# Kernel tuning notes

Hardware: AMD Instinct MI355X
Metric: run time of the kernel (lower is better)

The kernel has to match this reference:

```python
import jax, jax.numpy as jnp
import numpy as np

N_NODES = 7
SIZE_X = 27
SIZE_X0 = 23
SIZE_H = 1024
SIZE_Z = 256
BATCH = 2048


def _gru(x, h, Wih, Whh, bih, bhh):
    # torch.nn.GRUCell math
    gi = x @ Wih.T + bih          # [B, 3H]
    gh = h @ Whh.T + bhh          # [B, 3H]
    ir, iz, inn = jnp.split(gi, 3, axis=-1)
    hr, hz, hn = jnp.split(gh, 3, axis=-1)
    r = jax.nn.sigmoid(ir + hr)
    z = jax.nn.sigmoid(iz + hz)
    n = jnp.tanh(inn + r * hn)
    return (1.0 - z) * n + z * h


def setup_inputs() -> dict:
    key = jax.random.key(0)
    ks = jax.random.split(key, 24)
    H, Xd, X0d, Zd = SIZE_H, SIZE_X, SIZE_X0, SIZE_Z

    def w(k, shape, fan):
        return jax.random.normal(k, shape, jnp.float32) / np.float32(np.sqrt(fan))

    inp = {}
    inp['X'] = jax.random.normal(ks[0], (BATCH, N_NODES, Xd), jnp.float32)
    inp['adj'] = jax.random.randint(ks[1], (BATCH, N_NODES, N_NODES), 0, 2, jnp.int32)
    # combin_encode GRUCell
    inp['W_ih_c'] = w(ks[2], (3 * H, Xd), H)
    inp['W_hh_c'] = w(ks[3], (3 * H, H), H)
    inp['b_ih_c'] = w(ks[4], (3 * H,), H)
    inp['b_hh_c'] = w(ks[5], (3 * H,), H)
    # loop_encode GRUCell
    inp['W_ih_l'] = w(ks[6], (3 * H, Xd), H)
    inp['W_hh_l'] = w(ks[7], (3 * H, H), H)
    inp['b_ih_l'] = w(ks[8], (3 * H,), H)
    inp['b_hh_l'] = w(ks[9], (3 * H,), H)
    # root_encode GRUCell (input size = size_X0)
    inp['W_ih_r'] = w(ks[10], (3 * H, X0d), H)
    inp['W_hh_r'] = w(ks[11], (3 * H, H), H)
    inp['b_ih_r'] = w(ks[12], (3 * H,), H)
    inp['b_hh_r'] = w(ks[13], (3 * H,), H)
    # gate: Linear(2H -> H) + sigmoid ; mapper: Linear(2H -> H, no bias)
    inp['Wg'] = w(ks[14], (H, 2 * H), 2 * H)
    inp['bg'] = w(ks[15], (H,), 2 * H)
    inp['Wm'] = w(ks[16], (H, 2 * H), 2 * H)
    # h_to_mu, h_to_std (Linear(H -> Z), std with softplus)
    inp['Wmu'] = w(ks[17], (Zd, H), H)
    inp['bmu'] = w(ks[18], (Zd,), H)
    inp['Wstd'] = w(ks[19], (Zd, H), H)
    inp['bstd'] = w(ks[20], (Zd,), H)
    return inp


def reference(X, adj,
              W_ih_c, W_hh_c, b_ih_c, b_hh_c,
              W_ih_l, W_hh_l, b_ih_l, b_hh_l,
              W_ih_r, W_hh_r, b_ih_r, b_hh_r,
              Wg, bg, Wm, Wmu, bmu, Wstd, bstd):
    B = X.shape[0]
    hidden = jnp.zeros((B, N_NODES, SIZE_H), X.dtype)
    # encode: nodes processed v = n-1 .. 0 (fixed small unrolled loop)
    for v in range(N_NODES - 1, -1, -1):
        if v == N_NODES - 1:
            H_in = jnp.zeros((B, SIZE_H), X.dtype)  # H_init = zeros
        else:
            H_nb = hidden[:, v + 1:, :]                    # [B, k, H] neighbors v+1..n-1
            pred = (adj[:, v + 1:, v] > 0)[..., None]       # edge x -> v
            succ = (adj[:, v, v + 1:] > 0)[..., None]       # edge v -> x
            Hcat = jnp.concatenate([jnp.where(pred, H_nb, 0.0),
                                    jnp.where(succ, H_nb, 0.0)], axis=-1)  # [B, k, 2H]
            g = jax.nn.sigmoid(jnp.einsum('bkf,hf->bkh', Hcat, Wg) + bg)
            m = jnp.einsum('bkf,hf->bkh', Hcat, Wm)
            H_in = (g * m).sum(axis=1)                      # gated sum over neighbors
        Xv = X[:, v]
        if v == 0:
            Hv = _gru(Xv[:, :SIZE_X0], H_in, W_ih_r, W_hh_r, b_ih_r, b_hh_r)
        else:
            Hv = _gru(Xv, H_in, W_ih_c, W_hh_c, b_ih_c, b_hh_c)
            self_loop = (adj[:, v, v] > 0)[:, None]
            X_loop = jnp.where(self_loop, Xv, 0.0)
            Hv = _gru(X_loop, Hv, W_ih_l, W_hh_l, b_ih_l, b_hh_l)
        hidden = hidden.at[:, v].set(Hv)
    Hg = hidden[:, 0]
    mu = Hg @ Wmu.T + bmu
    std = jax.nn.softplus(Hg @ Wstd.T + bstd)
    return mu, std
```

## Files before the change

### kernel.cpp

```cpp
#include <hip/hip_runtime.h>
#include <hip/hip_bf16.h>
#include <cmath>


typedef __hip_bfloat16 bf16;
typedef __attribute__((ext_vector_type(8))) short bf16x8;
typedef __attribute__((ext_vector_type(4))) float f32x4;

constexpr int BATCH = 2048;
constexpr int HD    = 1024;
constexpr int LDA   = 1056;
constexpr size_t BH = (size_t)BATCH * HD;

__device__ __forceinline__ bf16  f2bf(float v){ return __float2bfloat16(v); }
__device__ __forceinline__ float sigm(float x){ return 1.0f/(1.0f+__expf(-x)); }

__device__ __forceinline__ void async16(bf16* lds_wave_uniform, const bf16* g){
  __builtin_amdgcn_global_load_lds(
      (const __attribute__((address_space(1))) void*)g,
      (__attribute__((address_space(3))) void*)lds_wave_uniform, 16, 0, 0);
}
__device__ __forceinline__ void ld4f(const bf16* p, float* o){
  ushort4 u = *reinterpret_cast<const ushort4*>(p);
  o[0] = __uint_as_float(((unsigned)u.x)<<16);
  o[1] = __uint_as_float(((unsigned)u.y)<<16);
  o[2] = __uint_as_float(((unsigned)u.z)<<16);
  o[3] = __uint_as_float(((unsigned)u.w)<<16);
}
__device__ __forceinline__ void st4bf(bf16* p, const float* v){
  bf16 o[4] = {f2bf(v[0]), f2bf(v[1]), f2bf(v[2]), f2bf(v[3])};
  *reinterpret_cast<ushort4*>(p) = *reinterpret_cast<const ushort4*>(o);
}

__global__ __launch_bounds__(256) void pack_waug_i(
    const float* __restrict__ Whh, const float* __restrict__ Wih, int xw,
    bf16* __restrict__ out)
{
  int c = blockIdx.x;
  int h = c >> 2, g = c & 3;
  for (int ch = threadIdx.x; ch < 264; ch += 256){
    int f0 = ch*4;
    float v[4] = {0.f,0.f,0.f,0.f};
    if (f0 < 1024){
      if (g < 3){
        int src = (g==2) ? (2048+h) : (g*1024+h);
        const float4 t = *reinterpret_cast<const float4*>(Whh + (size_t)src*1024 + f0);
        v[0]=t.x; v[1]=t.y; v[2]=t.z; v[3]=t.w;
      }
    } else if (g != 2){
      int src = (g==0) ? h : (g==1) ? (1024+h) : (2048+h);
      int fx = f0 - 1024;
      #pragma unroll
      for (int j=0;j<4;++j) if (fx+j < xw) v[j] = Wih[(size_t)src*xw + fx + j];
    }
    st4bf(out + (size_t)c*LDA + f0, v);
  }
}

__global__ __launch_bounds__(256) void pack_wgm(const float* __restrict__ Wg,
    const float* __restrict__ Wm, bf16* __restrict__ outW){
  int i = blockIdx.x*256 + threadIdx.x;
  int c = i >> 8, f0 = (i & 255)*4;
  int j = c >> 10, h = c & 1023;
  const float* src = (j < 2) ? Wg : Wm;
  float4 t = *reinterpret_cast<const float4*>(src + (size_t)h*2048 + ((j & 1) ? 1024 : 0) + f0);
  float v[4] = {t.x,t.y,t.z,t.w};
  st4bf(outW + (size_t)c*1024 + f0, v);
}

__global__ __launch_bounds__(256) void pack_wms(const float* __restrict__ Wmu,
    const float* __restrict__ Wstd, bf16* __restrict__ outW){
  int i = blockIdx.x*256 + threadIdx.x;
  int c = i >> 8, f0 = (i & 255)*4;
  const float* src = (c < 256) ? (Wmu + (size_t)c*1024) : (Wstd + (size_t)(c-256)*1024);
  float4 t = *reinterpret_cast<const float4*>(src + f0);
  float v[4] = {t.x,t.y,t.z,t.w};
  st4bf(outW + (size_t)c*1024 + f0, v);
}

__global__ __launch_bounds__(256) void pack_xpad(const float* __restrict__ X,
    bf16* __restrict__ out){
  int i = blockIdx.x*256 + threadIdx.x;
  int f = i & 31, bv = i >> 5;
  int b = bv / 7, v = bv % 7;
  float val = (f < 27) ? X[((size_t)b*7 + v)*27 + f] : 0.f;
  out[((size_t)v*BATCH + b)*32 + f] = f2bf(val);
}
__global__ __launch_bounds__(256) void pack_xpr(const float* __restrict__ X,
    bf16* __restrict__ out){
  int i = blockIdx.x*256 + threadIdx.x;
  int f = i & 31, b = i >> 5;
  float val = (f < 23) ? X[(size_t)b*7*27 + f] : 0.f;
  out[(size_t)b*32 + f] = f2bf(val);
}

__global__ __launch_bounds__(256) void combine_k(
    const bf16* __restrict__ P, const int* __restrict__ adj,
    const float* __restrict__ bg, const bf16* __restrict__ tailsrc,
    bf16* __restrict__ Hin, int v)
{
  int t  = threadIdx.x;
  int b  = blockIdx.x*2 + (t>>7);
  int tl = t & 127;
  int h0 = tl*8;
  float acc[8] = {0,0,0,0,0,0,0,0};
  float bgv[8];
  { const float4 a = *reinterpret_cast<const float4*>(bg + h0);
    const float4 c = *reinterpret_cast<const float4*>(bg + h0 + 4);
    bgv[0]=a.x;bgv[1]=a.y;bgv[2]=a.z;bgv[3]=a.w;bgv[4]=c.x;bgv[5]=c.y;bgv[6]=c.z;bgv[7]=c.w; }
  for (int k=v+1;k<7;++k){
    bool p = adj[b*49 + k*7 + v] > 0;
    bool s = adj[b*49 + v*7 + k] > 0;
    if (!p && !s) continue;
    const bf16* base = P + (size_t)(k-1)*4*BH + (size_t)b*HD + h0;
    float g1[8], g2[8], m1[8], m2[8];
    ld4f(base,          g1); ld4f(base+4,        g1+4);
    ld4f(base+BH,       g2); ld4f(base+BH+4,     g2+4);
    ld4f(base+2*BH,     m1); ld4f(base+2*BH+4,   m1+4);
    ld4f(base+3*BH,     m2); ld4f(base+3*BH+4,   m2+4);
    #pragma unroll
    for (int u=0;u<8;++u){
      float gg = (p?g1[u]:0.f) + (s?g2[u]:0.f);
      float mm = (p?m1[u]:0.f) + (s?m2[u]:0.f);
      acc[u] += sigm(gg + bgv[u]) * mm;
    }
  }
  st4bf(Hin + (size_t)b*LDA + h0,     acc);
  st4bf(Hin + (size_t)b*LDA + h0 + 4, acc+4);
  if (tl < 4){
    const ushort4* s0 = reinterpret_cast<const ushort4*>(tailsrc + (size_t)b*32 + tl*8);
    ushort4* d0 = reinterpret_cast<ushort4*>(Hin + (size_t)b*LDA + 1024 + tl*8);
    d0[0] = s0[0]; d0[1] = s0[1];
  }
}

template<int MODE>
__global__ __launch_bounds__(512, 4) void gemm_t(
    const bf16* __restrict__ A, const bf16* __restrict__ Bw,
    bf16* __restrict__ out, float* __restrict__ outF,
    const float* __restrict__ bias1, const float* __restrict__ bias2,
    const int* __restrict__ adj, const bf16* __restrict__ xpad,
    int lda, int ldb, int kb, int ktot, int v, int tailw, int swz)
{
  __shared__ __align__(16) bf16 S[32768];
  const int tid  = threadIdx.x;
  int bx, by;
  if (swz){ int xcd = blockIdx.x & 7, s = blockIdx.x >> 3;
    bx = ((xcd & 1) << 3) | (s & 7);
    by = ((xcd >> 1) << 3) | (s >> 3);
  } else { bx = blockIdx.x; by = blockIdx.y; }
  const int rb0  = bx*128, n0 = by*128;
  const int lane = tid & 63, w = tid >> 6;
  const int quad = lane >> 4, l15 = lane & 15;
  const int sr   = lane >> 2, sc = (lane & 3)*8;
  const int wr   = w >> 2,    wc = w & 3;

  const bf16* gA = A  + (size_t)(rb0 + w*16 + sr)*lda + sc;
  const bf16* gB = Bw + (size_t)(n0  + w*16 + sr)*ldb + sc;
  const int dA = w*512;
  const int dB = 4096 + w*512;

  const int nt = (ktot - kb + 63) >> 6;

  {
    async16(S + dA, gA + kb);
    async16(S + dB, gB + kb);
    if (ktot - kb > 32){
      async16(S + 8192 + dA, gA + kb + 32);
      async16(S + 8192 + dB, gB + kb + 32);
    }
  }
  __syncthreads();

  f32x4 acc[4][2] = {};
  for (int t = 0; t < nt; ++t){
    const int k0 = kb + t*64;
    if (t + 1 < nt){
      bf16* bp = S + ((t+1)&1)*16384;
      const int k1 = k0 + 64;
      async16(bp + dA, gA + k1);
      async16(bp + dB, gB + k1);
      if (ktot - k1 > 32){
        async16(bp + 8192 + dA, gA + k1 + 32);
        async16(bp + 8192 + dB, gB + k1 + 32);
      }
    }
    const bf16* buf = S + (t&1)*16384;
    {
      const bf16* As = buf;
      const bf16* Bs = buf + 4096;
      bf16x8 aa[4], bb[2];
      #pragma unroll
      for (int m=0;m<4;++m)
        aa[m] = *reinterpret_cast<const bf16x8*>(&As[(wr*64 + m*16 + l15)*32 + quad*8]);
      #pragma unroll
      for (int n=0;n<2;++n)
        bb[n] = *reinterpret_cast<const bf16x8*>(&Bs[(wc*32 + n*16 + l15)*32 + quad*8]);
      #pragma unroll
      for (int m=0;m<4;++m)
        #pragma unroll
        for (int n=0;n<2;++n)
          acc[m][n] = __builtin_amdgcn_mfma_f32_16x16x32_bf16(aa[m], bb[n], acc[m][n], 0,0,0);
    }
    if (ktot - k0 > 32){
      const bf16* As = buf + 8192;
      const bf16* Bs = buf + 12288;
      bf16x8 aa[4], bb[2];
      #pragma unroll
      for (int m=0;m<4;++m)
        aa[m] = *reinterpret_cast<const bf16x8*>(&As[(wr*64 + m*16 + l15)*32 + quad*8]);
      #pragma unroll
      for (int n=0;n<2;++n)
        bb[n] = *reinterpret_cast<const bf16x8*>(&Bs[(wc*32 + n*16 + l15)*32 + quad*8]);
      #pragma unroll
      for (int m=0;m<4;++m)
        #pragma unroll
        for (int n=0;n<2;++n)
          acc[m][n] = __builtin_amdgcn_mfma_f32_16x16x32_bf16(aa[m], bb[n], acc[m][n], 0,0,0);
    }
    __syncthreads();
  }

  if (MODE == 1 || MODE == 2){
    #pragma unroll
    for (int tm=0;tm<4;++tm)
      #pragma unroll
      for (int tn=0;tn<2;++tn)
        #pragma unroll
        for (int i=0;i<4;++i){
          int b = rb0 + wr*64 + tm*16 + quad*4 + i;
          int c = n0  + wc*32 + tn*16 + l15;
          float val = acc[tm][tn][i];
          if (MODE == 1){
            out[((size_t)(c>>10)*BATCH + b)*HD + (c & 1023)] = f2bf(val);
          } else {
            if (c < 256){
              outF[(size_t)b*256 + c] = val + bias1[c];
            } else {
              val += bias2[c-256];
              val = fmaxf(val,0.f) + log1pf(__expf(-fabsf(val)));
              outF[(size_t)BATCH*256 + (size_t)b*256 + (c-256)] = val;
            }
          }
        }
    return;
  }

  #pragma unroll
  for (int tm=0;tm<4;++tm)
    #pragma unroll
    for (int tn=0;tn<2;++tn)
      #pragma unroll
      for (int i=0;i<4;++i){
        int r = wr*64 + tm*16 + quad*4 + i;
        int c = wc*32 + tn*16 + l15;
        S[r*136 + c] = f2bf(acc[tm][tn][i]);
      }
  __syncthreads();
  {
    const int row = tid >> 2;
    const int hs  = (tid & 3)*8;
    const int b   = rb0 + row;
    const int hbase = by*32;
    bf16 hv[16];
    #pragma unroll
    for (int j4=0; j4<8; j4+=4){
      const int hg = hbase + hs + j4;
      float4 bir = *reinterpret_cast<const float4*>(bias1 + hg);
      float4 biz = *reinterpret_cast<const float4*>(bias1 + 1024 + hg);
      float4 bin = *reinterpret_cast<const float4*>(bias1 + 2048 + hg);
      float4 bhr = *reinterpret_cast<const float4*>(bias2 + hg);
      float4 bhz = *reinterpret_cast<const float4*>(bias2 + 1024 + hg);
      float4 bhn = *reinterpret_cast<const float4*>(bias2 + 2048 + hg);
      const float* p_ir = &bir.x; const float* p_iz = &biz.x; const float* p_in = &bin.x;
      const float* p_hr = &bhr.x; const float* p_hz = &bhz.x; const float* p_hn = &bhn.x;
      float ho[4];
      ld4f(A + (size_t)b*lda + hg, ho);
      #pragma unroll
      for (int jj=0; jj<4; ++jj){
        float g[4];
        ld4f(&S[row*136 + (hs + j4 + jj)*4], g);
        float r = sigm(g[0] + p_ir[jj] + p_hr[jj]);
        float z = sigm(g[1] + p_iz[jj] + p_hz[jj]);
        float n = tanhf(g[3] + p_in[jj] + r*(g[2] + p_hn[jj]));
        hv[j4+jj] = f2bf((1.f - z)*n + z*ho[jj]);
      }
    }
    *reinterpret_cast<uint4*>(out + (size_t)b*lda + hbase + hs) =
        *reinterpret_cast<const uint4*>(&hv[0]);
  }
  if (tailw && by == 0){
    const int b2 = rb0 + (tid>>2), f0 = (tid&3)*8;
    bool self = adj[b2*49 + v*8] > 0;
    uint4 tv = {0u,0u,0u,0u};
    if (self) tv = *reinterpret_cast<const uint4*>(xpad + (size_t)b2*32 + f0);
    *reinterpret_cast<uint4*>(out + (size_t)b2*lda + 1024 + f0) = tv;
  }
}

extern "C" void kernel_launch(void* const* d_in, const int* in_sizes, int n_in,
                              void* d_out, int out_size, void* d_ws, size_t ws_size,
                              hipStream_t stream)
{
  const float* X    = (const float*)d_in[0];
  const int*   adj  = (const int*)  d_in[1];
  const float* Wihc = (const float*)d_in[2];
  const float* Whhc = (const float*)d_in[3];
  const float* bihc = (const float*)d_in[4];
  const float* bhhc = (const float*)d_in[5];
  const float* Wihl = (const float*)d_in[6];
  const float* Whhl = (const float*)d_in[7];
  const float* bihl = (const float*)d_in[8];
  const float* bhhl = (const float*)d_in[9];
  const float* Wihr = (const float*)d_in[10];
  const float* Whhr = (const float*)d_in[11];
  const float* bihr = (const float*)d_in[12];
  const float* bhhr = (const float*)d_in[13];
  const float* Wg   = (const float*)d_in[14];
  const float* bg   = (const float*)d_in[15];
  const float* Wm   = (const float*)d_in[16];
  const float* Wmu  = (const float*)d_in[17];
  const float* bmu  = (const float*)d_in[18];
  const float* Wstd = (const float*)d_in[19];
  const float* bstd = (const float*)d_in[20];
  float* out = (float*)d_out;

  bf16* P    = (bf16*)d_ws;
  bf16* Hin  = P    + 24*BH;
  bf16* Hva  = Hin  + (size_t)BATCH*LDA;
  bf16* Hvb  = Hva  + (size_t)BATCH*LDA;
  bf16* Wca  = Hvb  + (size_t)BATCH*LDA;
  bf16* Wla  = Wca  + (size_t)4096*LDA;
  bf16* Wra  = Wla  + (size_t)4096*LDA;
  bf16* Wgm  = Wra  + (size_t)4096*LDA;
  bf16* Wms  = Wgm  + (size_t)4096*1024;
  bf16* Xp   = Wms  + (size_t)512*1024;
  bf16* XpR  = Xp   + (size_t)7*BATCH*32;

  pack_waug_i<<<4096, 256, 0, stream>>>(Whhc, Wihc, 27, Wca);
  pack_waug_i<<<4096, 256, 0, stream>>>(Whhl, Wihl, 27, Wla);
  pack_waug_i<<<4096, 256, 0, stream>>>(Whhr, Wihr, 23, Wra);
  pack_wgm  <<<4096, 256, 0, stream>>>(Wg, Wm, Wgm);
  pack_wms  <<<512,  256, 0, stream>>>(Wmu, Wstd, Wms);
  pack_xpad <<<1792, 256, 0, stream>>>(X, Xp);
  pack_xpr  <<<256,  256, 0, stream>>>(X, XpR);

  for (int v=6; v>=1; --v){
    const bf16* xt = Xp + (size_t)v*BATCH*32;
    combine_k<<<1024, 256, 0, stream>>>(P, adj, bg, xt, Hin, v);
    gemm_t<0><<<512, 512, 0, stream>>>(Hin, Wca, Hva, nullptr,
        bihc, bhhc, adj, xt, LDA, LDA, (v==6)?1024:0, 1056, v, 1, 1);
    gemm_t<0><<<512, 512, 0, stream>>>(Hva, Wla, Hvb, nullptr,
        bihl, bhhl, adj, nullptr, LDA, LDA, 0, 1056, v, 0, 1);
    gemm_t<1><<<512, 512, 0, stream>>>(Hvb, Wgm, P + (size_t)(v-1)*4*BH,
        nullptr, nullptr, nullptr, nullptr, nullptr, LDA, 1024, 0, 1024, 0, 0, 1);
  }
  combine_k<<<1024, 256, 0, stream>>>(P, adj, bg, XpR, Hin, 0);
  gemm_t<0><<<512, 512, 0, stream>>>(Hin, Wra, Hva, nullptr,
      bihr, bhhr, adj, nullptr, LDA, LDA, 0, 1056, 0, 0, 1);
  gemm_t<2><<<dim3(16,4), 512, 0, stream>>>(Hva, Wms, nullptr, out,
      bmu, bstd, nullptr, nullptr, LDA, 1024, 0, 1024, 0, 0, 0);
}
```

Measured before the change: 676.0 us.

## Split K across wave groups with 64x64 per-wave tiles and LDS reduction

The GEMM kernel now gives each of the eight waves a 64x64 output subtile. Two groups of four waves each handle one 32-wide K half of every 64-wide stage, replacing the old 64x32 subtiles that each covered the full K. Larger per-wave tiles reduce LDS fragment reads per MFMA. The cost is a cross-group reduction of the accumulators through LDS at the end, an extra barrier, and epilogues that run on only half the waves. Accumulator register use doubles, which may hurt occupancy under the existing launch bounds of (512, 4).

```diff
diff --git a/kernel.cpp b/kernel.cpp
--- a/kernel.cpp
+++ b/kernel.cpp
@@ -153,7 +153,8 @@
   const int lane = tid & 63, w = tid >> 6;
   const int quad = lane >> 4, l15 = lane & 15;
   const int sr   = lane >> 2, sc = (lane & 3)*8;
-  const int wr   = w >> 2,    wc = w & 3;
+  const int q    = w & 3, qr = q >> 1, qc = q & 1;
+  const int hk   = w >> 2;
 
   const bf16* gA = A  + (size_t)(rb0 + w*16 + sr)*lda + sc;
   const bf16* gB = Bw + (size_t)(n0  + w*16 + sr)*ldb + sc;
@@ -172,7 +173,7 @@
   }
   __syncthreads();
 
-  f32x4 acc[4][2] = {};
+  f32x4 acc[4][4] = {};
   for (int t = 0; t < nt; ++t){
     const int k0 = kb + t*64;
     if (t + 1 < nt){
@@ -185,77 +186,91 @@
         async16(bp + 8192 + dB, gB + k1 + 32);
       }
     }
-    const bf16* buf = S + (t&1)*16384;
-    {
-      const bf16* As = buf;
-      const bf16* Bs = buf + 4096;
-      bf16x8 aa[4], bb[2];
+    if (hk == 0 || (ktot - k0 > 32)){
+      const bf16* As = S + (t&1)*16384 + hk*8192;
+      const bf16* Bs = As + 4096;
+      bf16x8 aa[4], bb[4];
       #pragma unroll
       for (int m=0;m<4;++m)
-        aa[m] = *reinterpret_cast<const bf16x8*>(&As[(wr*64 + m*16 + l15)*32 + quad*8]);
-      #pragma unroll
-      for (int n=0;n<2;++n)
-        bb[n] = *reinterpret_cast<const bf16x8*>(&Bs[(wc*32 + n*16 + l15)*32 + quad*8]);
+        aa[m] = *reinterpret_cast<const bf16x8*>(&As[(qr*64 + m*16 + l15)*32 + quad*8]);
+      #pragma unroll
+      for (int n=0;n<4;++n)
+        bb[n] = *reinterpret_cast<const bf16x8*>(&Bs[(qc*64 + n*16 + l15)*32 + quad*8]);
       #pragma unroll
       for (int m=0;m<4;++m)
         #pragma unroll
-        for (int n=0;n<2;++n)
+        for (int n=0;n<4;++n)
           acc[m][n] = __builtin_amdgcn_mfma_f32_16x16x32_bf16(aa[m], bb[n], acc[m][n], 0,0,0);
     }
-    if (ktot - k0 > 32){
-      const bf16* As = buf + 8192;
-      const bf16* Bs = buf + 12288;
-      bf16x8 aa[4], bb[2];
+    __syncthreads();
+  }
+
+  {
+    float* Sf = reinterpret_cast<float*>(S);
+    const int base = q * 4096;
+    if (hk == 1){
       #pragma unroll
       for (int m=0;m<4;++m)
-        aa[m] = *reinterpret_cast<const bf16x8*>(&As[(wr*64 + m*16 + l15)*32 + quad*8]);
-      #pragma unroll
-      for (int n=0;n<2;++n)
-        bb[n] = *reinterpret_cast<const bf16x8*>(&Bs[(wc*32 + n*16 + l15)*32 + quad*8]);
+        #pragma unroll
+        for (int n=0;n<4;++n){
+          const int c  = n*16 + l15;
+          const int rr = ((m*16 + quad*4) + 4*l15) & 63;
+          *reinterpret_cast<f32x4*>(&Sf[base + c*64 + rr]) = acc[m][n];
+        }
+    }
+    __syncthreads();
+    if (hk == 0){
       #pragma unroll
       for (int m=0;m<4;++m)
         #pragma unroll
-        for (int n=0;n<2;++n)
-          acc[m][n] = __builtin_amdgcn_mfma_f32_16x16x32_bf16(aa[m], bb[n], acc[m][n], 0,0,0);
-    }
-    __syncthreads();
+        for (int n=0;n<4;++n){
+          const int c  = n*16 + l15;
+          const int rr = ((m*16 + quad*4) + 4*l15) & 63;
+          acc[m][n] += *reinterpret_cast<const f32x4*>(&Sf[base + c*64 + rr]);
+        }
+    }
   }
 
   if (MODE == 1 || MODE == 2){
+    if (hk == 0){
+      #pragma unroll
+      for (int tm=0;tm<4;++tm)
+        #pragma unroll
+        for (int tn=0;tn<4;++tn)
+          #pragma unroll
+          for (int i=0;i<4;++i){
+            int b = rb0 + qr*64 + tm*16 + quad*4 + i;
+            int c = n0  + qc*64 + tn*16 + l15;
+            float val = acc[tm][tn][i];
+            if (MODE == 1){
+              out[((size_t)(c>>10)*BATCH + b)*HD + (c & 1023)] = f2bf(val);
+            } else {
+              if (c < 256){
+                outF[(size_t)b*256 + c] = val + bias1[c];
+              } else {
+                val += bias2[c-256];
+                val = fmaxf(val,0.f) + log1pf(__expf(-fabsf(val)));
+                outF[(size_t)BATCH*256 + (size_t)b*256 + (c-256)] = val;
+              }
+            }
+          }
+    }
+    return;
+  }
+
+  __syncthreads();
+  if (hk == 0){
     #pragma unroll
     for (int tm=0;tm<4;++tm)
       #pragma unroll
-      for (int tn=0;tn<2;++tn)
+      for (int tn=0;tn<4;++tn)
         #pragma unroll
         for (int i=0;i<4;++i){
-          int b = rb0 + wr*64 + tm*16 + quad*4 + i;
-          int c = n0  + wc*32 + tn*16 + l15;
-          float val = acc[tm][tn][i];
-          if (MODE == 1){
-            out[((size_t)(c>>10)*BATCH + b)*HD + (c & 1023)] = f2bf(val);
-          } else {
-            if (c < 256){
-              outF[(size_t)b*256 + c] = val + bias1[c];
-            } else {
-              val += bias2[c-256];
-              val = fmaxf(val,0.f) + log1pf(__expf(-fabsf(val)));
-              outF[(size_t)BATCH*256 + (size_t)b*256 + (c-256)] = val;
-            }
-          }
+          int r = qr*64 + tm*16 + quad*4 + i;
+          int c = qc*64 + tn*16 + l15;
+          S[r*136 + c] = f2bf(acc[tm][tn][i]);
         }
-    return;
-  }
-
-  #pragma unroll
-  for (int tm=0;tm<4;++tm)
-    #pragma unroll
-    for (int tn=0;tn<2;++tn)
-      #pragma unroll
-      for (int i=0;i<4;++i){
-        int r = wr*64 + tm*16 + quad*4 + i;
-        int c = wc*32 + tn*16 + l15;
-        S[r*136 + c] = f2bf(acc[tm][tn][i]);
-      }
+  }
   __syncthreads();
   {
     const int row = tid >> 2;
```

New measurement: 710.5 us. +5.1%, slower.
